# Kernel optimization log

Measured on AMD Instinct MI355X. Metric: run time of the kernel, lower is better.

The kernel has to match this reference:

```python
import jax, jax.numpy as jnp
import numpy as np

B, S, DIM, H = 2, 2048, 1024, 16
DK = DIM // H  # 64
NEG = -10000000000.0


def setup_inputs() -> dict:
    key = jax.random.key(0)
    k1, k2, k3, k4, k5, k6 = jax.random.split(key, 6)
    dec_xs = jax.random.normal(k1, (B, S, DIM), dtype=jnp.float32)
    enc_xs = jax.random.normal(k2, (B, S, DIM), dtype=jnp.float32)
    mask = jax.random.randint(k3, (B, S, S), 0, 2, dtype=jnp.int32)
    # torch Linear weights: out = x @ W.T, bias=False
    sc = 1.0 / np.sqrt(DIM)
    Wq = jax.random.normal(k4, (DIM, DIM), dtype=jnp.float32) * sc
    Wkv = jax.random.normal(k5, (2 * DIM, DIM), dtype=jnp.float32) * sc
    Wo = jax.random.normal(k6, (DIM, DIM), dtype=jnp.float32) * sc
    return {"dec_xs": dec_xs, "enc_xs": enc_xs, "Wq": Wq, "Wkv": Wkv, "Wo": Wo, "mask": mask}


def reference(dec_xs, enc_xs, Wq, Wkv, Wo, mask):
    b, s, dim = enc_xs.shape
    qs = dec_xs @ Wq.T                      # [b,s,dim]  (dropout inactive in eval)
    kv = enc_xs @ Wkv.T                     # [b,s,2*dim]
    ks, vs = jnp.split(kv, 2, axis=-1)
    # head layout: view(b, s, dk, h) -- heads LAST, as in the original
    qs = qs.reshape(b, s, DK, H)
    ks = ks.reshape(b, s, DK, H)
    vs = vs.reshape(b, s, DK, H)
    scores = jnp.einsum('bqdh,bkdh->bqkh', qs, ks) / np.sqrt(DK)
    scores = jnp.where(mask[..., None] == 0, NEG, scores)
    weights = jax.nn.softmax(scores, axis=-2)  # softmax over key axis
    out = jnp.einsum('bqkh,bkdh->bqdh', weights, vs).reshape(b, s, dim)
    return out @ Wo.T
```

## Files before the change

kernel.cpp:

```cpp
#include <hip/hip_runtime.h>
#include <hip/hip_bf16.h>

#define BB 2
#define SS 2048
#define DIMM 1024
#define HH 16
#define DKK 64
#define QSCALE 0.18033688011112042592f

using bf16 = __hip_bfloat16;
typedef __attribute__((ext_vector_type(8))) short v8s;
typedef __attribute__((ext_vector_type(4))) short v4s;
typedef __attribute__((ext_vector_type(4))) float f32x4;
typedef __attribute__((ext_vector_type(16))) float f32x16;

using lds_u32 = __attribute__((address_space(3))) unsigned int;
using glb_u32 = const __attribute__((address_space(1))) unsigned int;

__device__ __forceinline__ void gload16(void* lds, const void* g) {
  __builtin_amdgcn_global_load_lds((glb_u32*)g, (lds_u32*)lds, 16, 0, 0);
}

__device__ __forceinline__ void cvt4(const float* __restrict__ s,
                                     bf16* __restrict__ d, int idx) {
  const float4 f = ((const float4*)s)[idx];
  bf16 t[4] = {__float2bfloat16(f.x), __float2bfloat16(f.y),
               __float2bfloat16(f.z), __float2bfloat16(f.w)};
  *(v4s*)(d + (size_t)idx * 4) = *(const v4s*)t;
}

__device__ __forceinline__ int cvt_pk_bf16(float lo, float hi) {
  int r;
  asm("v_cvt_pk_bf16_f32 %0, %1, %2" : "=v"(r) : "v"(lo), "v"(hi));
  return r;
}

__global__ __launch_bounds__(256) void convert_pack_kernel(
    const float* __restrict__ dec, const float* __restrict__ enc,
    const float* __restrict__ Wq, const float* __restrict__ Wkv,
    const float* __restrict__ Wo, const int* __restrict__ mask,
    bf16* __restrict__ decb, bf16* __restrict__ encb, bf16* __restrict__ Wqb,
    bf16* __restrict__ Wkvb, bf16* __restrict__ Wob,
    unsigned long long* __restrict__ mp) {
  const int gid = blockIdx.x * 256 + threadIdx.x;
  const int NT = 256 * 1024;
#pragma unroll
  for (int i = 0; i < 4; ++i) cvt4(dec, decb, gid + i * NT);
#pragma unroll
  for (int i = 0; i < 4; ++i) cvt4(enc, encb, gid + i * NT);
  cvt4(Wq, Wqb, gid);
#pragma unroll
  for (int i = 0; i < 2; ++i) cvt4(Wkv, Wkvb, gid + i * NT);
  {
    const int n = gid >> 8;
    const int c4 = (gid & 255) * 4;
    const int h = c4 >> 6, d0 = c4 & 63;
    const float* src = Wo + (size_t)n * DIMM + h;
    bf16 t[4];
#pragma unroll
    for (int i2 = 0; i2 < 4; ++i2)
      t[i2] = __float2bfloat16(src[(d0 + i2) * 16]);
    *(v4s*)(Wob + (size_t)n * DIMM + c4) = *(const v4s*)t;
  }
  const int lane = threadIdx.x & 63;
  const int wave_id = gid >> 6;
  for (int i = 0; i < 32; ++i) {
    const size_t w = (size_t)wave_id * 32 + i;
    const unsigned long long bm = __ballot(mask[w * 64 + lane] != 0);
    if (lane == 0) {
      const int bb = (int)(w >> 16);
      const int qq = (int)((w >> 5) & 2047);
      const int kc = (int)(w & 31);
      mp[((size_t)bb * 32 + kc) * SS + qq] = bm;
    }
  }
}

__global__ __launch_bounds__(256) void proj_gemm_kernel(
    const bf16* __restrict__ decb, const bf16* __restrict__ encb,
    const bf16* __restrict__ Wqb, const bf16* __restrict__ Wkvb,
    bf16* __restrict__ Qr, bf16* __restrict__ Kr, bf16* __restrict__ Vt) {
  __shared__ __align__(16) bf16 As[128][64];
  __shared__ __align__(16) bf16 Bs[128][64];
  const int t = threadIdx.x;
  const int wave = t >> 6, lane = t & 63;
  const int quad = lane >> 4, l15 = lane & 15;
  const int wm = (wave >> 1) * 64, wn = (wave & 1) * 64;
  const int bx = blockIdx.x;
  const int kind = bx >> 3;
  const int g = bx & 7;
  const int m0 = blockIdx.y * 128;

  const int lrow = lane >> 3;
  const int lcol = (lane & 7) * 8;

  const bf16* aptr[4];
  const bf16* bptr[4];
#pragma unroll
  for (int j = 0; j < 4; ++j) {
    const int r = (wave * 4 + j) * 8 + lrow;
    const int pw = (r & 63) * 16 + g * 2 + (r >> 6);
    if (kind == 0) {
      aptr[j] = decb + (size_t)(m0 + r) * DIMM + lcol;
      bptr[j] = Wqb + (size_t)pw * DIMM + lcol;
    } else if (kind == 1) {
      aptr[j] = encb + (size_t)(m0 + r) * DIMM + lcol;
      bptr[j] = Wkvb + (size_t)pw * DIMM + lcol;
    } else {
      aptr[j] = Wkvb + (size_t)(pw + DIMM) * DIMM + lcol;
      bptr[j] = encb + (size_t)(m0 + r) * DIMM + lcol;
    }
  }

  f32x4 acc[4][4] = {};

  for (int kc = 0; kc < DIMM; kc += 64) {
    __syncthreads();
#pragma unroll
    for (int j = 0; j < 4; ++j) {
      gload16(&As[(wave * 4 + j) * 8][0], aptr[j] + kc);
      gload16(&Bs[(wave * 4 + j) * 8][0], bptr[j] + kc);
    }
    __syncthreads();
#pragma unroll
    for (int ks = 0; ks < 2; ++ks) {
      v8s af[4], bfr[4];
#pragma unroll
      for (int i = 0; i < 4; ++i)
        af[i] = *(const v8s*)&As[wm + i * 16 + l15][ks * 32 + quad * 8];
#pragma unroll
      for (int j = 0; j < 4; ++j)
        bfr[j] = *(const v8s*)&Bs[wn + j * 16 + l15][ks * 32 + quad * 8];
#pragma unroll
      for (int i = 0; i < 4; ++i)
#pragma unroll
        for (int j = 0; j < 4; ++j)
          acc[i][j] = __builtin_amdgcn_mfma_f32_16x16x32_bf16(
              af[i], bfr[j], acc[i][j], 0, 0, 0);
    }
  }

#pragma unroll
  for (int i = 0; i < 4; ++i) {
#pragma unroll
    for (int r = 0; r < 4; ++r) {
      const int mm = wm + i * 16 + quad * 4 + r;
#pragma unroll
      for (int j = 0; j < 4; ++j) {
        const int nn = wn + j * 16 + l15;
        const float v = acc[i][j][r];
        if (kind == 0) {
          Qr[(size_t)(m0 + mm) * DIMM + g * 128 + nn] =
              __float2bfloat16(v * QSCALE);
        } else if (kind == 1) {
          Kr[(size_t)(m0 + mm) * DIMM + g * 128 + nn] = __float2bfloat16(v);
        } else {
          const int h = g * 2 + (mm >> 6), d = mm & 63;
          const int sn = m0 + nn;
          const int b = sn >> 11, s = sn & (SS - 1);
          Vt[(((size_t)b * HH + h) * DKK + d) * SS + s] = __float2bfloat16(v);
        }
      }
    }
  }
}

__global__ __launch_bounds__(256) void out_gemm_kernel(
    const bf16* __restrict__ A, const bf16* __restrict__ W,
    float* __restrict__ out) {
  __shared__ __align__(16) bf16 As[128][64];
  __shared__ __align__(16) bf16 Bs[64][64];
  const int t = threadIdx.x;
  const int wave = t >> 6, lane = t & 63;
  const int quad = lane >> 4, l15 = lane & 15;
  const int wm = (wave >> 1) * 64, wn = (wave & 1) * 32;
  const int n0 = blockIdx.x * 64;
  const int m0 = blockIdx.y * 128;

  const int lrow = lane >> 3;
  const int lcol = (lane & 7) * 8;

  const bf16* aptr[4];
  const bf16* bptr[2];
#pragma unroll
  for (int j = 0; j < 4; ++j)
    aptr[j] = A + (size_t)(m0 + (wave * 4 + j) * 8 + lrow) * DIMM + lcol;
#pragma unroll
  for (int j = 0; j < 2; ++j)
    bptr[j] = W + (size_t)(n0 + (wave * 2 + j) * 8 + lrow) * DIMM + lcol;

  f32x4 acc[4][2] = {};

  for (int kc = 0; kc < DIMM; kc += 64) {
    __syncthreads();
#pragma unroll
    for (int j = 0; j < 4; ++j)
      gload16(&As[(wave * 4 + j) * 8][0], aptr[j] + kc);
#pragma unroll
    for (int j = 0; j < 2; ++j)
      gload16(&Bs[(wave * 2 + j) * 8][0], bptr[j] + kc);
    __syncthreads();
#pragma unroll
    for (int ks = 0; ks < 2; ++ks) {
      v8s af[4], bfr[2];
#pragma unroll
      for (int i = 0; i < 4; ++i)
        af[i] = *(const v8s*)&As[wm + i * 16 + l15][ks * 32 + quad * 8];
#pragma unroll
      for (int j = 0; j < 2; ++j)
        bfr[j] = *(const v8s*)&Bs[wn + j * 16 + l15][ks * 32 + quad * 8];
#pragma unroll
      for (int i = 0; i < 4; ++i)
#pragma unroll
        for (int j = 0; j < 2; ++j)
          acc[i][j] = __builtin_amdgcn_mfma_f32_16x16x32_bf16(
              af[i], bfr[j], acc[i][j], 0, 0, 0);
    }
  }

#pragma unroll
  for (int i = 0; i < 4; ++i) {
#pragma unroll
    for (int r = 0; r < 4; ++r) {
      const int m = m0 + wm + i * 16 + quad * 4 + r;
#pragma unroll
      for (int j = 0; j < 2; ++j) {
        const int n = n0 + wn + j * 16 + l15;
        out[(size_t)m * DIMM + n] = acc[i][j][r];
      }
    }
  }
}

__global__ __launch_bounds__(512) void attn_kernel(
    const bf16* __restrict__ Qr, const bf16* __restrict__ Kr,
    const bf16* __restrict__ Vt, const unsigned long long* __restrict__ mp,
    bf16* __restrict__ Ar) {
  __shared__ __align__(16) bf16 smem[2][2][2][64][72];

  const int t = threadIdx.x;
  const int wave = t >> 6, lane = t & 63;
  const int l31 = lane & 31, hf = lane >> 5;
  const int qb = wave & 3;
  const int pr = wave >> 2;

  const int bx = blockIdx.x;
  const int xcd = bx & 7, j = bx >> 3;
  const int g = (xcd << 2) | (j & 3);
  const int tile = j >> 2;
  const int hd = g & 15, b = g >> 4;

  const int qw = tile * 128 + qb * 32;
  const size_t bhv = ((size_t)b * HH + hd) * DKK;

  v8s bq[4];
  {
    const bf16* qrow = Qr + ((size_t)(b * SS + qw + l31)) * DIMM + hd * 64;
#pragma unroll
    for (int cs = 0; cs < 4; ++cs)
      bq[cs] = *(const v8s*)(qrow + cs * 16 + 8 * hf);
  }

  v8s vones;
#pragma unroll
  for (int i = 0; i < 8; ++i) vones[i] = (short)0x3F80;

  f32x16 o0 = {}, o1 = {}, ol = {};

  const int r0 = t >> 3;
  const int c0 = (t & 7) * 8;

  auto gK = [&](int kt) {
    return *(const v8s*)(Kr + ((size_t)(b * SS + kt * 64 + r0)) * DIMM +
                         hd * 64 + c0);
  };
  auto gV = [&](int kt) {
    return *(const v8s*)(Vt + (bhv + r0) * SS + kt * 64 + c0);
  };
  auto loadM = [&](int kt) {
    return mp[((size_t)b * 32 + kt) * SS + qw + l31];
  };

  {
    const v8s k0 = gK(0), v0 = gV(0), k1 = gK(1), v1 = gV(1);
    *(v8s*)&smem[0][0][0][r0][c0] = k0;
    *(v8s*)&smem[1][0][0][r0][c0] = v0;
    *(v8s*)&smem[0][1][0][r0][c0] = k1;
    *(v8s*)&smem[1][1][0][r0][c0] = v1;
  }
  v8s kpr[2], vpr[2];
  kpr[0] = gK(2);
  vpr[0] = gV(2);
  kpr[1] = gK(3);
  vpr[1] = gV(3);
  unsigned long long mwcur = loadM(pr);

  for (int s = 0; s < 16; ++s) {
    __syncthreads();
    const int nb = (s + 1) & 1;
    if (s < 15) {
      *(v8s*)&smem[0][0][nb][r0][c0] = kpr[0];
      *(v8s*)&smem[1][0][nb][r0][c0] = vpr[0];
      *(v8s*)&smem[0][1][nb][r0][c0] = kpr[1];
      *(v8s*)&smem[1][1][nb][r0][c0] = vpr[1];
      if (s < 14) {
        kpr[0] = gK(2 * s + 4);
        vpr[0] = gV(2 * s + 4);
        kpr[1] = gK(2 * s + 5);
        vpr[1] = gV(2 * s + 5);
      }
    }
    const unsigned long long mwnext = (s < 15) ? loadM(2 * s + 2 + pr) : 0ULL;
    const unsigned long long mq = mwcur >> (4 * hf);
    const int cb = s & 1;

    f32x16 st[2];
#pragma unroll
    for (int n = 0; n < 2; ++n) {
      f32x16 sa = {};
#pragma unroll
      for (int cs = 0; cs < 4; ++cs) {
        const v8s ak =
            *(const v8s*)&smem[0][pr][cb][n * 32 + l31][cs * 16 + 8 * hf];
        sa = __builtin_amdgcn_mfma_f32_32x32x16_bf16(ak, bq[cs], sa, 0, 0, 0);
      }
      st[n] = sa;
    }

    int pd[8][2];
#pragma unroll
    for (int n = 0; n < 2; ++n)
#pragma unroll
      for (int g2 = 0; g2 < 4; ++g2)
#pragma unroll
        for (int jj = 0; jj < 2; ++jj) {
          const int bp = 32 * n + 8 * g2 + 2 * jj;
          const int m = g2 * 4 + 2 * jj;
          const float p0 =
              ((mq >> bp) & 1) ? __builtin_amdgcn_exp2f(st[n][m]) : 0.f;
          const float p1 =
              ((mq >> (bp + 1)) & 1) ? __builtin_amdgcn_exp2f(st[n][m + 1])
                                     : 0.f;
          pd[n * 4 + g2][jj] = cvt_pk_bf16(p0, p1);
        }

    v8s af[4];
#pragma unroll
    for (int ks = 0; ks < 4; ++ks) {
      int a0 = pd[2 * ks][0], b0 = pd[2 * ks + 1][0];
      int a1 = pd[2 * ks][1], b1 = pd[2 * ks + 1][1];
      asm("v_permlane32_swap_b32 %0, %1" : "+v"(a0), "+v"(b0));
      asm("v_permlane32_swap_b32 %0, %1" : "+v"(a1), "+v"(b1));
      int4 w;
      w.x = a0;
      w.y = a1;
      w.z = b0;
      w.w = b1;
      af[ks] = *(v8s*)&w;
    }

#pragma unroll
    for (int ks = 0; ks < 4; ++ks) {
      const v8s bv0 = *(const v8s*)&smem[1][pr][cb][l31][ks * 16 + 8 * hf];
      const v8s bv1 =
          *(const v8s*)&smem[1][pr][cb][32 + l31][ks * 16 + 8 * hf];
      o0 = __builtin_amdgcn_mfma_f32_32x32x16_bf16(af[ks], bv0, o0, 0, 0, 0);
      o1 = __builtin_amdgcn_mfma_f32_32x32x16_bf16(af[ks], bv1, o1, 0, 0, 0);
      ol = __builtin_amdgcn_mfma_f32_32x32x16_bf16(af[ks], vones, ol, 0, 0, 0);
    }
    mwcur = mwnext;
  }

  __syncthreads();
  float* scratch = (float*)&smem[0][0][0][0][0];
  if (wave >= 4) {
    float* dst = scratch + ((size_t)(wave - 4) * 64 + lane) * 52;
#pragma unroll
    for (int i = 0; i < 4; ++i) {
      f32x4 t0 = {o0[4 * i], o0[4 * i + 1], o0[4 * i + 2], o0[4 * i + 3]};
      f32x4 t1 = {o1[4 * i], o1[4 * i + 1], o1[4 * i + 2], o1[4 * i + 3]};
      f32x4 t2 = {ol[4 * i], ol[4 * i + 1], ol[4 * i + 2], ol[4 * i + 3]};
      *(f32x4*)(dst + 4 * i) = t0;
      *(f32x4*)(dst + 16 + 4 * i) = t1;
      *(f32x4*)(dst + 32 + 4 * i) = t2;
    }
  }
  __syncthreads();
  if (wave < 4) {
    const float* src = scratch + ((size_t)wave * 64 + lane) * 52;
#pragma unroll
    for (int m = 0; m < 16; ++m) {
      o0[m] += src[m];
      o1[m] += src[16 + m];
      ol[m] += src[32 + m];
    }
#pragma unroll
    for (int m = 0; m < 16; ++m) {
      const float inv = __builtin_amdgcn_rcpf(ol[m]);
      const int q = qw + (m & 3) + 8 * (m >> 2) + 4 * hf;
      const size_t row = (size_t)b * SS + q;
      Ar[row * DIMM + hd * 64 + l31] = __float2bfloat16(o0[m] * inv);
      Ar[row * DIMM + hd * 64 + 32 + l31] = __float2bfloat16(o1[m] * inv);
    }
  }
}

extern "C" void kernel_launch(void* const* d_in, const int* in_sizes, int n_in,
                              void* d_out, int out_size, void* d_ws,
                              size_t ws_size, hipStream_t stream) {
  const float* dec = (const float*)d_in[0];
  const float* enc = (const float*)d_in[1];
  const float* Wq = (const float*)d_in[2];
  const float* Wkv = (const float*)d_in[3];
  const float* Wo = (const float*)d_in[4];
  const int* mask = (const int*)d_in[5];
  float* out = (float*)d_out;

  bf16* decb = (bf16*)d_out;
  bf16* Wqb = (bf16*)((char*)d_out + ((size_t)2 * SS * DIMM * 2));

  char* ws = (char*)d_ws;
  size_t off = 0;
  bf16* encb = (bf16*)(ws + off);
  bf16* Ar = (bf16*)(ws + off);   off += (size_t)2 * SS * DIMM * 2;
  bf16* Wkvb = (bf16*)(ws + off); off += (size_t)2 * DIMM * DIMM * 2;
  bf16* Wob = (bf16*)(ws + off);  off += (size_t)DIMM * DIMM * 2;
  bf16* Qr = (bf16*)(ws + off);   off += (size_t)2 * SS * DIMM * 2;
  bf16* Kr = (bf16*)(ws + off);   off += (size_t)2 * SS * DIMM * 2;
  bf16* Vt = (bf16*)(ws + off);   off += (size_t)2 * SS * DIMM * 2;
  unsigned long long* mp = (unsigned long long*)(ws + off);

  dim3 blk(256);
  convert_pack_kernel<<<dim3(1024), blk, 0, stream>>>(
      dec, enc, Wq, Wkv, Wo, mask, decb, encb, Wqb, Wkvb, Wob, mp);
  proj_gemm_kernel<<<dim3(24, 32), blk, 0, stream>>>(decb, encb, Wqb, Wkvb, Qr,
                                                     Kr, Vt);
  attn_kernel<<<dim3(512), dim3(512), 0, stream>>>(Qr, Kr, Vt, mp, Ar);
  out_gemm_kernel<<<dim3(16, 32), blk, 0, stream>>>(Ar, Wob, out);
}
```

Before: 247.3 us.

## Split attention tiles into 64-query blocks with intra-tile key split across waves

Restructures the attention kernel from 512-thread blocks covering 128 queries to 256-thread blocks covering 64 queries, doubling the grid to 1024 blocks. Within a block, two wave pairs split each 64-key tile in half (32 keys each) instead of splitting alternate key tiles, and the loop now walks 32 single tiles with a smaller double-buffered LDS. The intent is better occupancy and load balance across CUs with less LDS per block. In exchange, each K/V tile is loaded by twice as many blocks, and each wave issues more barriers per unit of work.

```diff
diff --git a/kernel.cpp b/kernel.cpp
--- a/kernel.cpp
+++ b/kernel.cpp
@@ -232,25 +232,25 @@
   }
 }
 
-__global__ __launch_bounds__(512) void attn_kernel(
+__global__ __launch_bounds__(256, 4) void attn_kernel(
     const bf16* __restrict__ Qr, const bf16* __restrict__ Kr,
     const bf16* __restrict__ Vt, const unsigned long long* __restrict__ mp,
     bf16* __restrict__ Ar) {
-  __shared__ __align__(16) bf16 smem[2][2][2][64][72];
+  __shared__ __align__(16) bf16 smem[2][2][64][72];
 
   const int t = threadIdx.x;
   const int wave = t >> 6, lane = t & 63;
   const int l31 = lane & 31, hf = lane >> 5;
-  const int qb = wave & 3;
-  const int pr = wave >> 2;
+  const int qg = wave & 1;
+  const int kh = wave >> 1;
 
   const int bx = blockIdx.x;
   const int xcd = bx & 7, j = bx >> 3;
   const int g = (xcd << 2) | (j & 3);
-  const int tile = j >> 2;
+  const int t64 = j >> 2;
   const int hd = g & 15, b = g >> 4;
 
-  const int qw = tile * 128 + qb * 32;
+  const int qw = t64 * 64 + qg * 32;
   const size_t bhv = ((size_t)b * HH + hd) * DKK;
 
   v8s bq[4];
@@ -267,88 +267,79 @@
 
   f32x16 o0 = {}, o1 = {}, ol = {};
 
-  const int r0 = t >> 3;
-  const int c0 = (t & 7) * 8;
-
-  auto gK = [&](int kt) {
-    return *(const v8s*)(Kr + ((size_t)(b * SS + kt * 64 + r0)) * DIMM +
-                         hd * 64 + c0);
+  const int r0 = t >> 2;
+  const int c0 = (t & 3) * 16;
+
+  auto gK = [&](int kt, v8s* kr) {
+    const bf16* p =
+        Kr + ((size_t)(b * SS + kt * 64 + r0)) * DIMM + hd * 64 + c0;
+    kr[0] = ((const v8s*)p)[0];
+    kr[1] = ((const v8s*)p)[1];
   };
-  auto gV = [&](int kt) {
-    return *(const v8s*)(Vt + (bhv + r0) * SS + kt * 64 + c0);
+  auto gV = [&](int kt, v8s* vr) {
+    const bf16* p = Vt + (bhv + r0) * SS + kt * 64 + c0;
+    vr[0] = ((const v8s*)p)[0];
+    vr[1] = ((const v8s*)p)[1];
   };
   auto loadM = [&](int kt) {
     return mp[((size_t)b * 32 + kt) * SS + qw + l31];
   };
 
-  {
-    const v8s k0 = gK(0), v0 = gV(0), k1 = gK(1), v1 = gV(1);
-    *(v8s*)&smem[0][0][0][r0][c0] = k0;
-    *(v8s*)&smem[1][0][0][r0][c0] = v0;
-    *(v8s*)&smem[0][1][0][r0][c0] = k1;
-    *(v8s*)&smem[1][1][0][r0][c0] = v1;
-  }
-  v8s kpr[2], vpr[2];
-  kpr[0] = gK(2);
-  vpr[0] = gV(2);
-  kpr[1] = gK(3);
-  vpr[1] = gV(3);
-  unsigned long long mwcur = loadM(pr);
-
-  for (int s = 0; s < 16; ++s) {
+  v8s kreg[2], vreg[2];
+  gK(0, kreg);
+  gV(0, vreg);
+  *(v8s*)&smem[0][0][r0][c0] = kreg[0];
+  *(v8s*)&smem[0][0][r0][c0 + 8] = kreg[1];
+  *(v8s*)&smem[0][1][r0][c0] = vreg[0];
+  *(v8s*)&smem[0][1][r0][c0 + 8] = vreg[1];
+  gK(1, kreg);
+  gV(1, vreg);
+  unsigned long long mwcur = loadM(0);
+
+  for (int s = 0; s < 32; ++s) {
     __syncthreads();
     const int nb = (s + 1) & 1;
-    if (s < 15) {
-      *(v8s*)&smem[0][0][nb][r0][c0] = kpr[0];
-      *(v8s*)&smem[1][0][nb][r0][c0] = vpr[0];
-      *(v8s*)&smem[0][1][nb][r0][c0] = kpr[1];
-      *(v8s*)&smem[1][1][nb][r0][c0] = vpr[1];
-      if (s < 14) {
-        kpr[0] = gK(2 * s + 4);
-        vpr[0] = gV(2 * s + 4);
-        kpr[1] = gK(2 * s + 5);
-        vpr[1] = gV(2 * s + 5);
+    const int cb = s & 1;
+    if (s < 31) {
+      *(v8s*)&smem[nb][0][r0][c0] = kreg[0];
+      *(v8s*)&smem[nb][0][r0][c0 + 8] = kreg[1];
+      *(v8s*)&smem[nb][1][r0][c0] = vreg[0];
+      *(v8s*)&smem[nb][1][r0][c0 + 8] = vreg[1];
+      if (s < 30) {
+        gK(s + 2, kreg);
+        gV(s + 2, vreg);
       }
     }
-    const unsigned long long mwnext = (s < 15) ? loadM(2 * s + 2 + pr) : 0ULL;
+    const unsigned long long mwnext = (s < 31) ? loadM(s + 1) : 0ULL;
     const unsigned long long mq = mwcur >> (4 * hf);
-    const int cb = s & 1;
-
-    f32x16 st[2];
-#pragma unroll
-    for (int n = 0; n < 2; ++n) {
-      f32x16 sa = {};
-#pragma unroll
-      for (int cs = 0; cs < 4; ++cs) {
-        const v8s ak =
-            *(const v8s*)&smem[0][pr][cb][n * 32 + l31][cs * 16 + 8 * hf];
-        sa = __builtin_amdgcn_mfma_f32_32x32x16_bf16(ak, bq[cs], sa, 0, 0, 0);
+
+    f32x16 sa = {};
+#pragma unroll
+    for (int cs = 0; cs < 4; ++cs) {
+      const v8s ak =
+          *(const v8s*)&smem[cb][0][kh * 32 + l31][cs * 16 + 8 * hf];
+      sa = __builtin_amdgcn_mfma_f32_32x32x16_bf16(ak, bq[cs], sa, 0, 0, 0);
+    }
+
+    int pd[4][2];
+#pragma unroll
+    for (int g2 = 0; g2 < 4; ++g2)
+#pragma unroll
+      for (int jj = 0; jj < 2; ++jj) {
+        const int bp = 32 * kh + 8 * g2 + 2 * jj;
+        const int m = g2 * 4 + 2 * jj;
+        const float p0 =
+            ((mq >> bp) & 1) ? __builtin_amdgcn_exp2f(sa[m]) : 0.f;
+        const float p1 =
+            ((mq >> (bp + 1)) & 1) ? __builtin_amdgcn_exp2f(sa[m + 1]) : 0.f;
+        pd[g2][jj] = cvt_pk_bf16(p0, p1);
       }
-      st[n] = sa;
-    }
-
-    int pd[8][2];
-#pragma unroll
-    for (int n = 0; n < 2; ++n)
-#pragma unroll
-      for (int g2 = 0; g2 < 4; ++g2)
-#pragma unroll
-        for (int jj = 0; jj < 2; ++jj) {
-          const int bp = 32 * n + 8 * g2 + 2 * jj;
-          const int m = g2 * 4 + 2 * jj;
-          const float p0 =
-              ((mq >> bp) & 1) ? __builtin_amdgcn_exp2f(st[n][m]) : 0.f;
-          const float p1 =
-              ((mq >> (bp + 1)) & 1) ? __builtin_amdgcn_exp2f(st[n][m + 1])
-                                     : 0.f;
-          pd[n * 4 + g2][jj] = cvt_pk_bf16(p0, p1);
-        }
-
-    v8s af[4];
-#pragma unroll
-    for (int ks = 0; ks < 4; ++ks) {
-      int a0 = pd[2 * ks][0], b0 = pd[2 * ks + 1][0];
-      int a1 = pd[2 * ks][1], b1 = pd[2 * ks + 1][1];
+
+    v8s af[2];
+#pragma unroll
+    for (int kso = 0; kso < 2; ++kso) {
+      int a0 = pd[2 * kso][0], b0 = pd[2 * kso + 1][0];
+      int a1 = pd[2 * kso][1], b1 = pd[2 * kso + 1][1];
       asm("v_permlane32_swap_b32 %0, %1" : "+v"(a0), "+v"(b0));
       asm("v_permlane32_swap_b32 %0, %1" : "+v"(a1), "+v"(b1));
       int4 w;
@@ -356,25 +347,26 @@
       w.y = a1;
       w.z = b0;
       w.w = b1;
-      af[ks] = *(v8s*)&w;
-    }
-
-#pragma unroll
-    for (int ks = 0; ks < 4; ++ks) {
-      const v8s bv0 = *(const v8s*)&smem[1][pr][cb][l31][ks * 16 + 8 * hf];
-      const v8s bv1 =
-          *(const v8s*)&smem[1][pr][cb][32 + l31][ks * 16 + 8 * hf];
-      o0 = __builtin_amdgcn_mfma_f32_32x32x16_bf16(af[ks], bv0, o0, 0, 0, 0);
-      o1 = __builtin_amdgcn_mfma_f32_32x32x16_bf16(af[ks], bv1, o1, 0, 0, 0);
-      ol = __builtin_amdgcn_mfma_f32_32x32x16_bf16(af[ks], vones, ol, 0, 0, 0);
+      af[kso] = *(v8s*)&w;
+    }
+
+#pragma unroll
+    for (int kso = 0; kso < 2; ++kso) {
+      const int ks = 2 * kh + kso;
+      const v8s bv0 = *(const v8s*)&smem[cb][1][l31][ks * 16 + 8 * hf];
+      const v8s bv1 = *(const v8s*)&smem[cb][1][32 + l31][ks * 16 + 8 * hf];
+      o0 = __builtin_amdgcn_mfma_f32_32x32x16_bf16(af[kso], bv0, o0, 0, 0, 0);
+      o1 = __builtin_amdgcn_mfma_f32_32x32x16_bf16(af[kso], bv1, o1, 0, 0, 0);
+      ol = __builtin_amdgcn_mfma_f32_32x32x16_bf16(af[kso], vones, ol, 0, 0,
+                                                   0);
     }
     mwcur = mwnext;
   }
 
   __syncthreads();
-  float* scratch = (float*)&smem[0][0][0][0][0];
-  if (wave >= 4) {
-    float* dst = scratch + ((size_t)(wave - 4) * 64 + lane) * 52;
+  float* scratch = (float*)&smem[0][0][0][0];
+  if (kh == 1) {
+    float* dst = scratch + ((size_t)qg * 64 + lane) * 52;
 #pragma unroll
     for (int i = 0; i < 4; ++i) {
       f32x4 t0 = {o0[4 * i], o0[4 * i + 1], o0[4 * i + 2], o0[4 * i + 3]};
@@ -386,8 +378,8 @@
     }
   }
   __syncthreads();
-  if (wave < 4) {
-    const float* src = scratch + ((size_t)wave * 64 + lane) * 52;
+  if (kh == 0) {
+    const float* src = scratch + ((size_t)qg * 64 + lane) * 52;
 #pragma unroll
     for (int m = 0; m < 16; ++m) {
       o0[m] += src[m];
@@ -435,6 +427,6 @@
       dec, enc, Wq, Wkv, Wo, mask, decb, encb, Wqb, Wkvb, Wob, mp);
   proj_gemm_kernel<<<dim3(24, 32), blk, 0, stream>>>(decb, encb, Wqb, Wkvb, Qr,
                                                      Kr, Vt);
-  attn_kernel<<<dim3(512), dim3(512), 0, stream>>>(Qr, Kr, Vt, mp, Ar);
+  attn_kernel<<<dim3(1024), dim3(256), 0, stream>>>(Qr, Kr, Vt, mp, Ar);
   out_gemm_kernel<<<dim3(16, 32), blk, 0, stream>>>(Ar, Wob, out);
 }
```

New measurement: 296.7 us. 20.0% more time.

## Double-buffer LDS in projection and output GEMMs, remap blocks for XCD locality

Applied to the files above, without the earlier changes.

Both GEMM kernels now use two LDS buffers, so the tile for the next K step is loaded asynchronously while MFMAs run on the current one, and one barrier per iteration is dropped. Blocks are launched on a 1D grid and remapped so blocks sharing the same A rows land on the same XCD, which should improve L2 reuse. The output GEMM tile also grows from 128x64 to 128x128. This cuts its block count to 256 and raises per-block work and LDS use, which may reduce occupancy and leave some CUs underused.

```diff
diff --git a/kernel.cpp b/kernel.cpp
--- a/kernel.cpp
+++ b/kernel.cpp
@@ -80,16 +80,19 @@
     const bf16* __restrict__ decb, const bf16* __restrict__ encb,
     const bf16* __restrict__ Wqb, const bf16* __restrict__ Wkvb,
     bf16* __restrict__ Qr, bf16* __restrict__ Kr, bf16* __restrict__ Vt) {
-  __shared__ __align__(16) bf16 As[128][64];
-  __shared__ __align__(16) bf16 Bs[128][64];
+  __shared__ __align__(16) bf16 As[2][128][64];
+  __shared__ __align__(16) bf16 Bs[2][128][64];
   const int t = threadIdx.x;
   const int wave = t >> 6, lane = t & 63;
   const int quad = lane >> 4, l15 = lane & 15;
   const int wm = (wave >> 1) * 64, wn = (wave & 1) * 64;
-  const int bx = blockIdx.x;
-  const int kind = bx >> 3;
-  const int g = bx & 7;
-  const int m0 = blockIdx.y * 128;
+
+  const int bid = blockIdx.x;
+  const int xcd = bid & 7, slot = bid >> 3;
+  const int km = xcd + 8 * (slot >> 3);
+  const int g = slot & 7;
+  const int kind = km >> 5;
+  const int m0 = (km & 31) * 128;
 
   const int lrow = lane >> 3;
   const int lcol = (lane & 7) * 8;
@@ -112,25 +115,30 @@
     }
   }
 
+  auto stage = [&](int kc, int buf) {
+#pragma unroll
+    for (int j = 0; j < 4; ++j) {
+      gload16(&As[buf][(wave * 4 + j) * 8][0], aptr[j] + kc);
+      gload16(&Bs[buf][(wave * 4 + j) * 8][0], bptr[j] + kc);
+    }
+  };
+
   f32x4 acc[4][4] = {};
-
-  for (int kc = 0; kc < DIMM; kc += 64) {
+  stage(0, 0);
+
+  for (int kt = 0; kt < 16; ++kt) {
+    const int cb = kt & 1;
     __syncthreads();
-#pragma unroll
-    for (int j = 0; j < 4; ++j) {
-      gload16(&As[(wave * 4 + j) * 8][0], aptr[j] + kc);
-      gload16(&Bs[(wave * 4 + j) * 8][0], bptr[j] + kc);
-    }
-    __syncthreads();
+    if (kt < 15) stage((kt + 1) * 64, cb ^ 1);
 #pragma unroll
     for (int ks = 0; ks < 2; ++ks) {
       v8s af[4], bfr[4];
 #pragma unroll
       for (int i = 0; i < 4; ++i)
-        af[i] = *(const v8s*)&As[wm + i * 16 + l15][ks * 32 + quad * 8];
+        af[i] = *(const v8s*)&As[cb][wm + i * 16 + l15][ks * 32 + quad * 8];
 #pragma unroll
       for (int j = 0; j < 4; ++j)
-        bfr[j] = *(const v8s*)&Bs[wn + j * 16 + l15][ks * 32 + quad * 8];
+        bfr[j] = *(const v8s*)&Bs[cb][wn + j * 16 + l15][ks * 32 + quad * 8];
 #pragma unroll
       for (int i = 0; i < 4; ++i)
 #pragma unroll
@@ -168,51 +176,58 @@
 __global__ __launch_bounds__(256) void out_gemm_kernel(
     const bf16* __restrict__ A, const bf16* __restrict__ W,
     float* __restrict__ out) {
-  __shared__ __align__(16) bf16 As[128][64];
-  __shared__ __align__(16) bf16 Bs[64][64];
+  __shared__ __align__(16) bf16 As[2][128][64];
+  __shared__ __align__(16) bf16 Bs[2][128][64];
   const int t = threadIdx.x;
   const int wave = t >> 6, lane = t & 63;
   const int quad = lane >> 4, l15 = lane & 15;
-  const int wm = (wave >> 1) * 64, wn = (wave & 1) * 32;
-  const int n0 = blockIdx.x * 64;
-  const int m0 = blockIdx.y * 128;
+  const int wm = (wave >> 1) * 64, wn = (wave & 1) * 64;
+
+  const int bid = blockIdx.x;
+  const int xcd = bid & 7, slot = bid >> 3;
+  const int m0 = (xcd + 8 * (slot >> 3)) * 128;
+  const int n0 = (slot & 7) * 128;
 
   const int lrow = lane >> 3;
   const int lcol = (lane & 7) * 8;
 
   const bf16* aptr[4];
-  const bf16* bptr[2];
-#pragma unroll
-  for (int j = 0; j < 4; ++j)
-    aptr[j] = A + (size_t)(m0 + (wave * 4 + j) * 8 + lrow) * DIMM + lcol;
-#pragma unroll
-  for (int j = 0; j < 2; ++j)
-    bptr[j] = W + (size_t)(n0 + (wave * 2 + j) * 8 + lrow) * DIMM + lcol;
-
-  f32x4 acc[4][2] = {};
-
-  for (int kc = 0; kc < DIMM; kc += 64) {
+  const bf16* bptr[4];
+#pragma unroll
+  for (int j = 0; j < 4; ++j) {
+    const int r = (wave * 4 + j) * 8 + lrow;
+    aptr[j] = A + (size_t)(m0 + r) * DIMM + lcol;
+    bptr[j] = W + (size_t)(n0 + r) * DIMM + lcol;
+  }
+
+  auto stage = [&](int kc, int buf) {
+#pragma unroll
+    for (int j = 0; j < 4; ++j) {
+      gload16(&As[buf][(wave * 4 + j) * 8][0], aptr[j] + kc);
+      gload16(&Bs[buf][(wave * 4 + j) * 8][0], bptr[j] + kc);
+    }
+  };
+
+  f32x4 acc[4][4] = {};
+  stage(0, 0);
+
+  for (int kt = 0; kt < 16; ++kt) {
+    const int cb = kt & 1;
     __syncthreads();
-#pragma unroll
-    for (int j = 0; j < 4; ++j)
-      gload16(&As[(wave * 4 + j) * 8][0], aptr[j] + kc);
-#pragma unroll
-    for (int j = 0; j < 2; ++j)
-      gload16(&Bs[(wave * 2 + j) * 8][0], bptr[j] + kc);
-    __syncthreads();
+    if (kt < 15) stage((kt + 1) * 64, cb ^ 1);
 #pragma unroll
     for (int ks = 0; ks < 2; ++ks) {
-      v8s af[4], bfr[2];
+      v8s af[4], bfr[4];
 #pragma unroll
       for (int i = 0; i < 4; ++i)
-        af[i] = *(const v8s*)&As[wm + i * 16 + l15][ks * 32 + quad * 8];
-#pragma unroll
-      for (int j = 0; j < 2; ++j)
-        bfr[j] = *(const v8s*)&Bs[wn + j * 16 + l15][ks * 32 + quad * 8];
+        af[i] = *(const v8s*)&As[cb][wm + i * 16 + l15][ks * 32 + quad * 8];
+#pragma unroll
+      for (int j = 0; j < 4; ++j)
+        bfr[j] = *(const v8s*)&Bs[cb][wn + j * 16 + l15][ks * 32 + quad * 8];
 #pragma unroll
       for (int i = 0; i < 4; ++i)
 #pragma unroll
-        for (int j = 0; j < 2; ++j)
+        for (int j = 0; j < 4; ++j)
           acc[i][j] = __builtin_amdgcn_mfma_f32_16x16x32_bf16(
               af[i], bfr[j], acc[i][j], 0, 0, 0);
     }
@@ -224,7 +239,7 @@
     for (int r = 0; r < 4; ++r) {
       const int m = m0 + wm + i * 16 + quad * 4 + r;
 #pragma unroll
-      for (int j = 0; j < 2; ++j) {
+      for (int j = 0; j < 4; ++j) {
         const int n = n0 + wn + j * 16 + l15;
         out[(size_t)m * DIMM + n] = acc[i][j][r];
       }
@@ -433,8 +448,8 @@
   dim3 blk(256);
   convert_pack_kernel<<<dim3(1024), blk, 0, stream>>>(
       dec, enc, Wq, Wkv, Wo, mask, decb, encb, Wqb, Wkvb, Wob, mp);
-  proj_gemm_kernel<<<dim3(24, 32), blk, 0, stream>>>(decb, encb, Wqb, Wkvb, Qr,
-                                                     Kr, Vt);
+  proj_gemm_kernel<<<dim3(768), blk, 0, stream>>>(decb, encb, Wqb, Wkvb, Qr,
+                                                  Kr, Vt);
   attn_kernel<<<dim3(512), dim3(512), 0, stream>>>(Qr, Kr, Vt, mp, Ar);
-  out_gemm_kernel<<<dim3(16, 32), blk, 0, stream>>>(Ar, Wob, out);
-}
+  out_gemm_kernel<<<dim3(256), blk, 0, stream>>>(Ar, Wob, out);
+}
```

Measured after the change: 268.2 us. 8.5% more time.
